# Optimization experiments

Hardware: AMD Instinct MI355X
Metric: run time of the kernel (lower is better)

## Reference

```python
import jax, jax.numpy as jnp
import numpy as np

B, S, I, H, O = 32, 4096, 64, 128, 64

def setup_inputs() -> dict:
    key = jax.random.key(0)
    ks = jax.random.split(key, 4)
    xavier_in = float(np.sqrt(6.0 / (I + H)))
    xavier_t3 = float(np.sqrt(6.0 / (H + H * H)))  # xavier_uniform_ on (H, H*H)-shaped fan view of (H,H,H)
    xavier_out = float(np.sqrt(6.0 / (H + O)))
    return {
        "u": jax.random.normal(ks[0], (B, S, I), dtype=jnp.float32),
        "hidden": jnp.zeros((B, H), dtype=jnp.float32),
        "W_in": jax.random.uniform(ks[1], (H, I), dtype=jnp.float32, minval=-xavier_in, maxval=xavier_in),
        "b_in": jnp.zeros((H,), dtype=jnp.float32),
        "T3": jax.random.uniform(ks[2], (H, H, H), dtype=jnp.float32, minval=-xavier_t3, maxval=xavier_t3),
        "bias_t": jnp.zeros((H,), dtype=jnp.float32),
        "W_out": jax.random.uniform(ks[3], (O, H), dtype=jnp.float32, minval=-xavier_out, maxval=xavier_out),
        "b_out": jnp.zeros((O,), dtype=jnp.float32),
    }

def reference(u, hidden, W_in, b_in, T3, bias_t, W_out, b_out):
    # Precompute input projection for all timesteps: [S, B, H]
    input_w = jnp.einsum('bsi,hi->sbh', u, W_in) + b_in

    def step(h, iw_t):
        # bilinear hidden-hidden contraction: out[b,i] = sum_{j,k} h[b,j] T3[i,j,k] h[b,k]
        hw = jnp.einsum('bj,ijk,bk->bi', h, T3, h) + bias_t
        h_new = jnp.tanh(hw + iw_t)
        return h_new, h_new

    h_last, r = jax.lax.scan(step, hidden, input_w)  # r: [S, B, H]
    r_out = jnp.transpose(r, (1, 0, 2))              # [B, S, H]
    output = jnp.einsum('bsh,oh->bso', r_out, W_out) + b_out
    return output, h_last, r_out
```

## Files before the change

kernel.cpp:

```cpp
#include <hip/hip_runtime.h>
#include <math.h>
#include <stdint.h>

#define NB 32
#define NS 4096
#define NI 64
#define NH 128
#define NO 64
#define RT 256

#define SPIN_MAX1 (1 << 24)
#define SPIN_MAX2 (1 << 22)

#define CH_STRIDE 12
#define B_STRIDE (16 * CH_STRIDE)

typedef float f4 __attribute__((ext_vector_type(4)));
typedef unsigned int u4 __attribute__((ext_vector_type(4)));

__global__ __launch_bounds__(256)
void k_input_proj(const float* __restrict__ u, const float* __restrict__ W_in,
                  const float* __restrict__ b_in, float* __restrict__ iw)
{
    const int gid = blockIdx.x * 256 + threadIdx.x;
    const int h = gid & (NH - 1);
    const int t = (gid >> 7) & (NS - 1);
    const int b = gid >> 19;
    const f4* ur = reinterpret_cast<const f4*>(u + ((size_t)b * NS + t) * NI);
    const f4* wr = reinterpret_cast<const f4*>(W_in + h * NI);
    float acc = b_in[h];
#pragma unroll
    for (int q = 0; q < NI / 4; ++q) {
        const f4 uv = ur[q], wv = wr[q];
        acc = fmaf(uv[0], wv[0], acc); acc = fmaf(uv[1], wv[1], acc);
        acc = fmaf(uv[2], wv[2], acc); acc = fmaf(uv[3], wv[3], acc);
    }
    iw[gid] = acc;
}

__global__ __launch_bounds__(256)
void k_init_hex(const float* __restrict__ hidden, uint64_t* __restrict__ hex)
{
    const int gid = blockIdx.x * 256 + threadIdx.x;
    const int b = gid & (NB - 1);
    const int i = gid >> 5;
    hex[gid] = (uint64_t)__float_as_uint(hidden[b * NH + i]);
}

__global__ __launch_bounds__(RT)
__attribute__((amdgpu_waves_per_eu(1, 1)))
void k_recur(const float* __restrict__ T3, const float* __restrict__ bias_t,
             float* __restrict__ r_region,
             float* __restrict__ h_last,
             uint64_t* hex)
{
    const int bi  = blockIdx.x;
    const int i   = bi >> 1;
    const int bh  = bi & 1;
    const int B0  = bh * 16;
    const int tid = threadIdx.x;
    const int jg  = tid >> 4;
    const int kg  = tid & 15;
    const int w   = tid >> 6;

    const int ipol = tid >> 1;
    const int oct  = 2 * bh + (tid & 1);
    const int bl0  = (tid & 1) * 8;

    __shared__ float h_lds[16 * B_STRIDE];
    __shared__ float redbuf[4][16];
    __shared__ float lds_pad[20480];

    const float* base = T3 + (size_t)i * NH * NH + (size_t)(jg * 8) * NH + kg * 8;
    f4 t3_0, t3_1, t3_2, t3_3, t3_4, t3_5, t3_6, t3_7;
    f4 t3_8, t3_9, t3_10, t3_11, t3_12, t3_13, t3_14, t3_15;
#define T3LOAD(dst, fofs) \
    asm volatile("global_load_dwordx4 %0, %1, off" \
                 : "=v"(dst) : "v"(base + (fofs)) : "memory")
    T3LOAD(t3_0,  0 * NH);     T3LOAD(t3_1,  0 * NH + 4);
    T3LOAD(t3_2,  1 * NH);     T3LOAD(t3_3,  1 * NH + 4);
    T3LOAD(t3_4,  2 * NH);     T3LOAD(t3_5,  2 * NH + 4);
    T3LOAD(t3_6,  3 * NH);     T3LOAD(t3_7,  3 * NH + 4);
    T3LOAD(t3_8,  4 * NH);     T3LOAD(t3_9,  4 * NH + 4);
    T3LOAD(t3_10, 5 * NH);     T3LOAD(t3_11, 5 * NH + 4);
    T3LOAD(t3_12, 6 * NH);     T3LOAD(t3_13, 6 * NH + 4);
    T3LOAD(t3_14, 7 * NH);     T3LOAD(t3_15, 7 * NH + 4);
#undef T3LOAD
    asm volatile("s_waitcnt vmcnt(0)" ::: "memory");
    __builtin_amdgcn_sched_barrier(0);

    const float bias = bias_t[i];
    if (bias > 1.0e30f) lds_pad[tid] = bias;

    float iw_cur = 0.f;
    if (tid < 16)
        iw_cur = r_region[((size_t)(B0 + tid) * NS + 0) * NH + i];

    for (int t = 0; t < NS; ++t) {
        {
            const uint64_t* src = hex + ((size_t)(t & 1) * NH + ipol) * NB + oct * 8;
            const uint32_t et = (uint32_t)t;
            uint64_t s0v;
            for (int spin = 0;; ++spin) {
                asm volatile("global_load_dwordx2 %0, %1, off sc0 sc1\n\t"
                             "s_waitcnt vmcnt(0)"
                             : "=v"(s0v) : "v"(src) : "memory");
                if (((uint32_t)(s0v >> 32) == et) | (spin > SPIN_MAX1)) break;
            }
            u4 q0, q1, q2, q3;
            for (int spin = 0;; ++spin) {
                asm volatile(
                    "global_load_dwordx4 %0, %4, off sc0 sc1\n\t"
                    "global_load_dwordx4 %1, %4, off offset:16 sc0 sc1\n\t"
                    "global_load_dwordx4 %2, %4, off offset:32 sc0 sc1\n\t"
                    "global_load_dwordx4 %3, %4, off offset:48 sc0 sc1\n\t"
                    "s_waitcnt vmcnt(0)"
                    : "=&v"(q0), "=&v"(q1), "=&v"(q2), "=&v"(q3)
                    : "v"(src) : "memory");
                if ((q0[1] == et && q0[3] == et && q1[1] == et && q1[3] == et &&
                     q2[1] == et && q2[3] == et && q3[1] == et && q3[3] == et)
                    | (spin > SPIN_MAX2))
                    break;
                asm volatile("s_sleep 1");
            }
            float* dst = h_lds + bl0 * B_STRIDE
                       + (ipol >> 3) * CH_STRIDE + (ipol & 7);
            dst[0 * B_STRIDE] = __uint_as_float(q0[0]);
            dst[1 * B_STRIDE] = __uint_as_float(q0[2]);
            dst[2 * B_STRIDE] = __uint_as_float(q1[0]);
            dst[3 * B_STRIDE] = __uint_as_float(q1[2]);
            dst[4 * B_STRIDE] = __uint_as_float(q2[0]);
            dst[5 * B_STRIDE] = __uint_as_float(q2[2]);
            dst[6 * B_STRIDE] = __uint_as_float(q3[0]);
            dst[7 * B_STRIDE] = __uint_as_float(q3[2]);
        }
        __syncthreads();

#define JJBODY(tA, tB, HJV) \
        { float s0 = 0.f, s1 = 0.f; \
          s0 = fmaf(tA[0], hk0[0], s0); s1 = fmaf(tA[1], hk0[1], s1); \
          s0 = fmaf(tA[2], hk0[2], s0); s1 = fmaf(tA[3], hk0[3], s1); \
          s0 = fmaf(tB[0], hk1[0], s0); s1 = fmaf(tB[1], hk1[1], s1); \
          s0 = fmaf(tB[2], hk1[2], s0); s1 = fmaf(tB[3], hk1[3], s1); \
          acc = fmaf(HJV, s0 + s1, acc); }
#pragma unroll 4
        for (int b = 0; b < 16; ++b) {
            const float* row = h_lds + b * B_STRIDE;
            const f4 hj0 = *reinterpret_cast<const f4*>(row + jg * CH_STRIDE);
            const f4 hj1 = *reinterpret_cast<const f4*>(row + jg * CH_STRIDE + 4);
            const f4 hk0 = *reinterpret_cast<const f4*>(row + kg * CH_STRIDE);
            const f4 hk1 = *reinterpret_cast<const f4*>(row + kg * CH_STRIDE + 4);
            float acc = 0.f;
            JJBODY(t3_0,  t3_1,  hj0[0]);
            JJBODY(t3_2,  t3_3,  hj0[1]);
            JJBODY(t3_4,  t3_5,  hj0[2]);
            JJBODY(t3_6,  t3_7,  hj0[3]);
            JJBODY(t3_8,  t3_9,  hj1[0]);
            JJBODY(t3_10, t3_11, hj1[1]);
            JJBODY(t3_12, t3_13, hj1[2]);
            JJBODY(t3_14, t3_15, hj1[3]);
            acc += __shfl_xor(acc, 1);  acc += __shfl_xor(acc, 2);
            acc += __shfl_xor(acc, 4);  acc += __shfl_xor(acc, 8);
            acc += __shfl_xor(acc, 16); acc += __shfl_xor(acc, 32);
            if ((tid & 63) == b) redbuf[w][b] = acc;
        }
#undef JJBODY
        __syncthreads();

        if (tid < 16) {
            const int b = B0 + tid;
            const float s = redbuf[0][tid] + redbuf[1][tid]
                          + redbuf[2][tid] + redbuf[3][tid];
            const float hn = tanhf(s + bias + iw_cur);
            const uint64_t pv = ((uint64_t)(uint32_t)(t + 1) << 32)
                              | (uint64_t)__float_as_uint(hn);
            uint64_t* dstp = hex + ((size_t)((t + 1) & 1) * NH + i) * NB + b;
            asm volatile("global_store_dwordx2 %0, %1, off sc0 sc1"
                         :: "v"(dstp), "v"(pv) : "memory");
            const size_t ridx = ((size_t)b * NS + t) * NH + i;
            r_region[ridx] = hn;
            if (t + 1 < NS) iw_cur = r_region[ridx + NH];
            if (t == NS - 1) h_last[(size_t)b * NH + i] = hn;
        }
    }
}

__global__ __launch_bounds__(256)
void k_out_proj(const float* __restrict__ r, const float* __restrict__ W_out,
                const float* __restrict__ b_out, float* __restrict__ out)
{
    const int gid = blockIdx.x * 256 + threadIdx.x;
    const int o = gid & (NO - 1);
    const int s = (gid >> 6) & (NS - 1);
    const int b = gid >> 18;
    const f4* rr = reinterpret_cast<const f4*>(r + ((size_t)b * NS + s) * NH);
    const f4* wr = reinterpret_cast<const f4*>(W_out + o * NH);
    float acc = b_out[o];
#pragma unroll
    for (int q = 0; q < NH / 4; ++q) {
        const f4 rv = rr[q], wv = wr[q];
        acc = fmaf(rv[0], wv[0], acc); acc = fmaf(rv[1], wv[1], acc);
        acc = fmaf(rv[2], wv[2], acc); acc = fmaf(rv[3], wv[3], acc);
    }
    out[gid] = acc;
}

extern "C" void kernel_launch(void* const* d_in, const int* in_sizes, int n_in,
                              void* d_out, int out_size, void* d_ws, size_t ws_size,
                              hipStream_t stream)
{
    const float* u      = (const float*)d_in[0];
    const float* hidden = (const float*)d_in[1];
    const float* W_in   = (const float*)d_in[2];
    const float* b_in   = (const float*)d_in[3];
    const float* T3     = (const float*)d_in[4];
    const float* bias_t = (const float*)d_in[5];
    const float* W_out  = (const float*)d_in[6];
    const float* b_out  = (const float*)d_in[7];

    float* out_f  = (float*)d_out;
    float* out_y  = out_f;
    float* out_hl = out_f + (size_t)NB * NS * NO;
    float* out_r  = out_hl + (size_t)NB * NH;

    uint64_t* hex = (uint64_t*)d_ws;

    hipMemsetAsync(hex, 0xFF, 2 * NB * NH * sizeof(uint64_t), stream);
    k_init_hex<<<(NB * NH) / 256, 256, 0, stream>>>(hidden, hex);

    k_input_proj<<<(NB * NS * NH) / 256, 256, 0, stream>>>(u, W_in, b_in, out_r);
    k_recur<<<2 * NH, RT, 0, stream>>>(T3, bias_t, out_r, out_hl, hex);
    k_out_proj<<<(NB * NS * NO) / 256, 256, 0, stream>>>(out_r, W_out, b_out, out_y);
}
```

Measured before the change: 36.22 ms.

## Replace per-thread flag polling with sharded atomic step counters

Adds counters in the workspace, split into four shards per batch half. Each block atomically increments its shard after publishing its hidden values for the step. Before reading the exchange buffer, four threads per block spin on the shard counters until all 128 producers have arrived, followed by a block barrier. This replaces the first polling loop, in which every thread spun on a tagged 64-bit word, and is meant to cut global polling traffic. In exchange it adds an atomic, an extra vmcnt wait and one more __syncthreads per step on the serial critical path, and it keeps the tagged-data verification loop.

```diff
diff --git a/kernel.cpp b/kernel.cpp
--- a/kernel.cpp
+++ b/kernel.cpp
@@ -52,7 +52,8 @@
 void k_recur(const float* __restrict__ T3, const float* __restrict__ bias_t,
              float* __restrict__ r_region,
              float* __restrict__ h_last,
-             uint64_t* hex)
+             uint64_t* hex,
+             uint32_t* cnts)
 {
     const int bi  = blockIdx.x;
     const int i   = bi >> 1;
@@ -96,17 +97,25 @@
     if (tid < 16)
         iw_cur = r_region[((size_t)(B0 + tid) * NS + 0) * NH + i];
 
+    uint32_t* cnt_my = cnts + (size_t)(bh * 4 + (i & 3)) * 16;
+
     for (int t = 0; t < NS; ++t) {
+        const uint32_t et = (uint32_t)t;
+        if (tid < 4) {
+            const uint32_t* cp = cnts + (size_t)(bh * 4 + tid) * 16;
+            const uint32_t tgt = 32u * et;
+            uint32_t v;
+            for (int spin = 0;; ++spin) {
+                asm volatile("global_load_dword %0, %1, off sc0 sc1\n\t"
+                             "s_waitcnt vmcnt(0)"
+                             : "=v"(v) : "v"(cp) : "memory");
+                if ((v >= tgt) | (spin > SPIN_MAX1)) break;
+            }
+        }
+        __syncthreads();
+
         {
             const uint64_t* src = hex + ((size_t)(t & 1) * NH + ipol) * NB + oct * 8;
-            const uint32_t et = (uint32_t)t;
-            uint64_t s0v;
-            for (int spin = 0;; ++spin) {
-                asm volatile("global_load_dwordx2 %0, %1, off sc0 sc1\n\t"
-                             "s_waitcnt vmcnt(0)"
-                             : "=v"(s0v) : "v"(src) : "memory");
-                if (((uint32_t)(s0v >> 32) == et) | (spin > SPIN_MAX1)) break;
-            }
             u4 q0, q1, q2, q3;
             for (int spin = 0;; ++spin) {
                 asm volatile(
@@ -167,20 +176,30 @@
 #undef JJBODY
         __syncthreads();
 
+        float hn = 0.f;
+        size_t ridx = 0;
         if (tid < 16) {
             const int b = B0 + tid;
             const float s = redbuf[0][tid] + redbuf[1][tid]
                           + redbuf[2][tid] + redbuf[3][tid];
-            const float hn = tanhf(s + bias + iw_cur);
+            hn = tanhf(s + bias + iw_cur);
+            ridx = ((size_t)b * NS + t) * NH + i;
             const uint64_t pv = ((uint64_t)(uint32_t)(t + 1) << 32)
                               | (uint64_t)__float_as_uint(hn);
             uint64_t* dstp = hex + ((size_t)((t + 1) & 1) * NH + i) * NB + b;
             asm volatile("global_store_dwordx2 %0, %1, off sc0 sc1"
                          :: "v"(dstp), "v"(pv) : "memory");
-            const size_t ridx = ((size_t)b * NS + t) * NH + i;
+        }
+        if (tid < 64) {
+            asm volatile("s_waitcnt vmcnt(0)" ::: "memory");
+            if (tid == 0)
+                __hip_atomic_fetch_add(cnt_my, 1u, __ATOMIC_RELAXED,
+                                       __HIP_MEMORY_SCOPE_SYSTEM);
+        }
+        if (tid < 16) {
             r_region[ridx] = hn;
             if (t + 1 < NS) iw_cur = r_region[ridx + NH];
-            if (t == NS - 1) h_last[(size_t)b * NH + i] = hn;
+            if (t == NS - 1) h_last[(size_t)(B0 + tid) * NH + i] = hn;
         }
     }
 }
@@ -223,12 +242,14 @@
     float* out_hl = out_f + (size_t)NB * NS * NO;
     float* out_r  = out_hl + (size_t)NB * NH;
 
-    uint64_t* hex = (uint64_t*)d_ws;
+    uint64_t* hex  = (uint64_t*)d_ws;
+    uint32_t* cnts = (uint32_t*)((char*)d_ws + 65536);
 
     hipMemsetAsync(hex, 0xFF, 2 * NB * NH * sizeof(uint64_t), stream);
+    hipMemsetAsync(cnts, 0, 512, stream);
     k_init_hex<<<(NB * NH) / 256, 256, 0, stream>>>(hidden, hex);
 
     k_input_proj<<<(NB * NS * NH) / 256, 256, 0, stream>>>(u, W_in, b_in, out_r);
-    k_recur<<<2 * NH, RT, 0, stream>>>(T3, bias_t, out_r, out_hl, hex);
+    k_recur<<<2 * NH, RT, 0, stream>>>(T3, bias_t, out_r, out_hl, hex, cnts);
     k_out_proj<<<(NB * NS * NO) / 256, 256, 0, stream>>>(out_r, W_out, b_out, out_y);
 }
```

Result: slower. 39.70 ms (+9.6%).
